# Optimization experiments

Hardware: AMD Instinct MI355X
Metric: run time of the kernel (lower is better)

The kernel has to match this reference:

```python
import jax, jax.numpy as jnp
import numpy as np

B, T, C, H = 2, 2048, 1024, 16
HD = C // H  # head_size = 64
EPS = 1e-5


def setup_inputs() -> dict:
    key = jax.random.key(0)
    ks = jax.random.split(key, 12)
    s = lambda fan_in: 1.0 / np.sqrt(fan_in)
    return {
        "x": jax.random.normal(ks[0], (B, T, C), jnp.float32),
        # attention projections, stored [in, out] so y = x @ W
        "Wq": jax.random.normal(ks[1], (C, C), jnp.float32) * s(C),
        "Wk": jax.random.normal(ks[2], (C, C), jnp.float32) * s(C),
        "Wv": jax.random.normal(ks[3], (C, C), jnp.float32) * s(C),
        "Wo": jax.random.normal(ks[4], (C, C), jnp.float32) * s(C),
        "bo": jnp.zeros((C,), jnp.float32),
        "ln1_g": jnp.ones((C,), jnp.float32),
        "ln1_b": jnp.zeros((C,), jnp.float32),
        "ln2_g": jnp.ones((C,), jnp.float32),
        "ln2_b": jnp.zeros((C,), jnp.float32),
        "W1": jax.random.normal(ks[5], (C, 4 * C), jnp.float32) * s(C),
        "b1": jnp.zeros((4 * C,), jnp.float32),
        "W2": jax.random.normal(ks[6], (4 * C, C), jnp.float32) * s(4 * C),
        "b2": jnp.zeros((C,), jnp.float32),
    }


def _layernorm(x, g, b):
    mu = jnp.mean(x, axis=-1, keepdims=True)
    var = jnp.mean(jnp.square(x - mu), axis=-1, keepdims=True)
    return (x - mu) * jax.lax.rsqrt(var + EPS) * g + b


def reference(x, Wq, Wk, Wv, Wo, bo, ln1_g, ln1_b, ln2_g, ln2_b, W1, b1, W2, b2):
    # Dropout layers are inference no-ops (eval mode).
    Bz, Tz, Cz = x.shape
    h = _layernorm(x, ln1_g, ln1_b)
    # fused multi-head projections (equivalent to per-head Linears concatenated)
    q = (h @ Wq).reshape(Bz, Tz, H, HD)
    k = (h @ Wk).reshape(Bz, Tz, H, HD)
    v = (h @ Wv).reshape(Bz, Tz, H, HD)
    scores = jnp.einsum("bqhd,bkhd->bhqk", q, k) / np.sqrt(HD).astype(np.float32)
    causal = jnp.tril(jnp.ones((Tz, Tz), bool))
    scores = jnp.where(causal, scores, -jnp.inf)
    attn = jax.nn.softmax(scores, axis=-1)
    out = jnp.einsum("bhqk,bkhd->bqhd", attn, v).reshape(Bz, Tz, Cz)
    x = x + out @ Wo + bo
    h2 = _layernorm(x, ln2_g, ln2_b)
    ff = jax.nn.relu(h2 @ W1 + b1) @ W2 + b2
    return x + ff
```

## Files before the change

kernel.cpp:

```cpp
#include <hip/hip_runtime.h>
#include <hip/hip_bf16.h>
#include <stdint.h>

#define B_  2
#define T_  2048
#define C_  1024
#define H_  16
#define HD_ 64
#define M_  4096
#define FF_ 4096

typedef unsigned short ushort_t;
typedef __bf16 bf16x8 __attribute__((ext_vector_type(8)));
typedef float  f32x4  __attribute__((ext_vector_type(4)));

__device__ inline ushort_t f2bf(float f) {
  uint32_t u = __builtin_bit_cast(uint32_t, f);
  u += 0x7fffu + ((u >> 16) & 1u);
  return (ushort_t)(u >> 16);
}

__device__ inline void gload_lds16(const void* g, void* l) {
  __builtin_amdgcn_global_load_lds(
      (const __attribute__((address_space(1))) uint32_t*)g,
      (__attribute__((address_space(3))) uint32_t*)l, 16, 0, 0);
}

__device__ inline int qswz(int row, int byte_in_row) {
  return row * 128 + (byte_in_row ^ ((row & 7) << 4));
}
__device__ inline int vswz(int row, int byte_in_row) {
  return row * 128 + (byte_in_row ^ (((row >> 3) & 7) << 4));
}

__global__ __launch_bounds__(256) void lnorm_kernel(
    const float* __restrict__ x, const float* __restrict__ g,
    const float* __restrict__ b, ushort_t* __restrict__ o) {
  int row = blockIdx.x;
  int tid = threadIdx.x;
  const float4* xr = (const float4*)(x + (size_t)row * C_);
  float4 xv = xr[tid];
  float s  = xv.x + xv.y + xv.z + xv.w;
  float s2 = xv.x*xv.x + xv.y*xv.y + xv.z*xv.z + xv.w*xv.w;
#pragma unroll
  for (int off = 32; off; off >>= 1) {
    s  += __shfl_down(s,  off);
    s2 += __shfl_down(s2, off);
  }
  __shared__ float rs[4], rq[4];
  int wid = tid >> 6;
  if ((tid & 63) == 0) { rs[wid] = s; rq[wid] = s2; }
  __syncthreads();
  float tot  = rs[0] + rs[1] + rs[2] + rs[3];
  float tot2 = rq[0] + rq[1] + rq[2] + rq[3];
  float mu   = tot * (1.0f / C_);
  float var  = tot2 * (1.0f / C_) - mu * mu;
  float rstd = rsqrtf(var + 1e-5f);
  float4 gv = ((const float4*)g)[tid];
  float4 bv = ((const float4*)b)[tid];
  float y0 = (xv.x - mu) * rstd * gv.x + bv.x;
  float y1 = (xv.y - mu) * rstd * gv.y + bv.y;
  float y2 = (xv.z - mu) * rstd * gv.z + bv.z;
  float y3 = (xv.w - mu) * rstd * gv.w + bv.w;
  uint2 pk;
  pk.x = (uint32_t)f2bf(y0) | ((uint32_t)f2bf(y1) << 16);
  pk.y = (uint32_t)f2bf(y2) | ((uint32_t)f2bf(y3) << 16);
  *(uint2*)(o + (size_t)row * C_ + tid * 4) = pk;
}

__global__ __launch_bounds__(256) void tcast_kernel(
    const float* __restrict__ W, ushort_t* __restrict__ Wt, int K, int N) {
  __shared__ float t[32][33];
  int bn = blockIdx.x, bk = blockIdx.y;
  int tx = threadIdx.x & 31, ty = threadIdx.x >> 5;
#pragma unroll
  for (int i = 0; i < 4; ++i)
    t[ty + i*8][tx] = W[(size_t)(bk*32 + ty + i*8) * N + bn*32 + tx];
  __syncthreads();
#pragma unroll
  for (int i = 0; i < 4; ++i)
    Wt[(size_t)(bn*32 + ty + i*8) * K + bk*32 + tx] = f2bf(t[tx][ty + i*8]);
}

template<int BIAS, int RELU, int RESID, int OUTBF16>
__global__ __launch_bounds__(256) void gemm_kernel(
    const ushort_t* __restrict__ A, const ushort_t* __restrict__ Bt,
    const float* __restrict__ bias, const float* __restrict__ resid,
    void* __restrict__ outp, int M, int N, int K) {
  __shared__ __align__(16) ushort_t As[128*32];
  __shared__ __align__(16) ushort_t Bs[128*32];
  int bn = blockIdx.x, bm = blockIdx.y;
  int tid = threadIdx.x;
  int lane = tid & 63, wid = tid >> 6;
  int wr = (wid >> 1) * 64, wc = (wid & 1) * 64;
  int r = lane & 15, g = lane >> 4;
  int srow = tid >> 2, scc = (tid & 3) * 8;
  int srow2 = srow + 64;
  f32x4 acc[4][4] = {};
  int nk = K >> 5;
  for (int kt = 0; kt < nk; ++kt) {
    gload_lds16(&A[(size_t)(bm*128 + srow)  * K + kt*32 + scc], &As[tid*8]);
    gload_lds16(&A[(size_t)(bm*128 + srow2) * K + kt*32 + scc], &As[(tid+256)*8]);
    gload_lds16(&Bt[(size_t)(bn*128 + srow)  * K + kt*32 + scc], &Bs[tid*8]);
    gload_lds16(&Bt[(size_t)(bn*128 + srow2) * K + kt*32 + scc], &Bs[(tid+256)*8]);
    __syncthreads();
    bf16x8 af[4], bfv[4];
#pragma unroll
    for (int m = 0; m < 4; ++m)
      af[m] = *(const bf16x8*)&As[(wr + m*16 + r)*32 + g*8];
#pragma unroll
    for (int n = 0; n < 4; ++n)
      bfv[n] = *(const bf16x8*)&Bs[(wc + n*16 + r)*32 + g*8];
#pragma unroll
    for (int m = 0; m < 4; ++m)
#pragma unroll
      for (int n = 0; n < 4; ++n)
        acc[m][n] = __builtin_amdgcn_mfma_f32_16x16x32_bf16(
            af[m], bfv[n], acc[m][n], 0, 0, 0);
    __syncthreads();
  }
#pragma unroll
  for (int m = 0; m < 4; ++m)
#pragma unroll
    for (int n = 0; n < 4; ++n)
#pragma unroll
      for (int e = 0; e < 4; ++e) {
        int row = bm*128 + wr + m*16 + g*4 + e;
        int col = bn*128 + wc + n*16 + r;
        float v = acc[m][n][e];
        if (BIAS)  v += bias[col];
        if (RESID) v += resid[(size_t)row * N + col];
        if (RELU)  v = fmaxf(v, 0.0f);
        if (OUTBF16) ((ushort_t*)outp)[(size_t)row * N + col] = f2bf(v);
        else         ((float*)outp)[(size_t)row * N + col]    = v;
      }
}

__global__ __launch_bounds__(256) void attn_kernel(
    const ushort_t* __restrict__ q, const ushort_t* __restrict__ k,
    const ushort_t* __restrict__ v, ushort_t* __restrict__ o, int ldq) {
  int bid = blockIdx.x;
  int qb = 31 - (bid & 31);
  int hh = (bid >> 5) & 15;
  int bb = bid >> 9;
  __shared__ __align__(16) ushort_t Qs[64*64], Ks[64*64], Vt[64*64];
  __shared__ __align__(16) ushort_t Ps[4][16*64];
  int tid = threadIdx.x, lane = tid & 63, w = tid >> 6;
  int r = lane & 15, g = lane >> 4;
#pragma unroll
  for (int p = 0; p < 2; ++p) {
    int ci = p*256 + tid;
    int row = ci >> 3, c8 = (ci & 7) * 8;
    *(uint4*)((char*)Qs + qswz(row, c8*2)) =
        *(const uint4*)&q[((size_t)(bb*T_ + qb*64 + row))*ldq + hh*64 + c8];
  }
  f32x4 O[4] = {};
  float mrow[4], lrow[4];
#pragma unroll
  for (int e = 0; e < 4; ++e) { mrow[e] = -1e30f; lrow[e] = 0.f; }
  for (int kb = 0; kb <= qb; ++kb) {
    __syncthreads();
#pragma unroll
    for (int p = 0; p < 2; ++p) {
      int ci = p*256 + tid;
      int row = ci >> 3, c8 = (ci & 7) * 8;
      *(uint4*)((char*)Ks + qswz(row, c8*2)) =
          *(const uint4*)&k[((size_t)(bb*T_ + kb*64 + row))*ldq + hh*64 + c8];
      int key = row;
      uint4 vv = *(const uint4*)&v[((size_t)(bb*T_ + kb*64 + key))*ldq + hh*64 + c8];
      ushort_t tmp[8];
      *(uint4*)tmp = vv;
#pragma unroll
      for (int j = 0; j < 8; ++j)
        *(ushort_t*)((char*)Vt + vswz(c8 + j, key*2)) = tmp[j];
    }
    __syncthreads();
    f32x4 s[4] = {};
#pragma unroll
    for (int ks = 0; ks < 2; ++ks) {
      bf16x8 aq = *(const bf16x8*)((char*)Qs + qswz(w*16 + r, (ks*32 + g*8)*2));
#pragma unroll
      for (int n = 0; n < 4; ++n) {
        bf16x8 bk = *(const bf16x8*)((char*)Ks + qswz(n*16 + r, (ks*32 + g*8)*2));
        s[n] = __builtin_amdgcn_mfma_f32_16x16x32_bf16(aq, bk, s[n], 0, 0, 0);
      }
    }
    int qrow0 = qb*64 + w*16 + g*4;
#pragma unroll
    for (int e = 0; e < 4; ++e) {
      float mx = -1e30f;
#pragma unroll
      for (int n = 0; n < 4; ++n) {
        float sv = s[n][e] * 0.125f;
        if (kb*64 + n*16 + r > qrow0 + e) sv = -1e30f;
        s[n][e] = sv;
        mx = fmaxf(mx, sv);
      }
#pragma unroll
      for (int off = 1; off < 16; off <<= 1)
        mx = fmaxf(mx, __shfl_xor(mx, off, 16));
      float mnew = fmaxf(mrow[e], mx);
      float sf = __expf(mrow[e] - mnew);
      mrow[e] = mnew;
      float rsum = 0.f;
#pragma unroll
      for (int n = 0; n < 4; ++n) {
        float p = __expf(s[n][e] - mnew);
        rsum += p;
        *(ushort_t*)((char*)&Ps[w][0] + qswz(g*4 + e, (n*16 + r)*2)) = f2bf(p);
      }
#pragma unroll
      for (int off = 1; off < 16; off <<= 1)
        rsum += __shfl_xor(rsum, off, 16);
      lrow[e] = lrow[e] * sf + rsum;
#pragma unroll
      for (int dn = 0; dn < 4; ++dn) O[dn][e] *= sf;
    }
    __syncthreads();
#pragma unroll
    for (int ks = 0; ks < 2; ++ks) {
      bf16x8 ap = *(const bf16x8*)((char*)&Ps[w][0] + qswz(r, (ks*32 + g*8)*2));
#pragma unroll
      for (int dn = 0; dn < 4; ++dn) {
        bf16x8 bv = *(const bf16x8*)((char*)Vt + vswz(dn*16 + r, (ks*32 + g*8)*2));
        O[dn] = __builtin_amdgcn_mfma_f32_16x16x32_bf16(ap, bv, O[dn], 0, 0, 0);
      }
    }
  }
#pragma unroll
  for (int dn = 0; dn < 4; ++dn)
#pragma unroll
    for (int e = 0; e < 4; ++e) {
      int tok = qb*64 + w*16 + g*4 + e;
      int col = hh*64 + dn*16 + r;
      o[((size_t)(bb*T_ + tok))*C_ + col] = f2bf(O[dn][e] / lrow[e]);
    }
}

extern "C" void kernel_launch(void* const* d_in, const int* in_sizes, int n_in,
                              void* d_out, int out_size, void* d_ws, size_t ws_size,
                              hipStream_t stream) {
  const float* x    = (const float*)d_in[0];
  const float* Wq   = (const float*)d_in[1];
  const float* Wk   = (const float*)d_in[2];
  const float* Wv   = (const float*)d_in[3];
  const float* Wo   = (const float*)d_in[4];
  const float* bo   = (const float*)d_in[5];
  const float* ln1g = (const float*)d_in[6];
  const float* ln1b = (const float*)d_in[7];
  const float* ln2g = (const float*)d_in[8];
  const float* ln2b = (const float*)d_in[9];
  const float* W1   = (const float*)d_in[10];
  const float* b1   = (const float*)d_in[11];
  const float* W2   = (const float*)d_in[12];
  const float* b2   = (const float*)d_in[13];

  char* ws = (char*)d_ws;
  ushort_t* h    = (ushort_t*)(ws + ((size_t)0  << 20));
  ushort_t* qkv  = (ushort_t*)(ws + ((size_t)8  << 20));
  ushort_t* ff   = (ushort_t*)(ws + ((size_t)0  << 20));
  ushort_t* attn = (ushort_t*)(ws + ((size_t)32 << 20));
  float*    x2   = (float*)   (ws + ((size_t)40 << 20));
  ushort_t* h2   = (ushort_t*)(ws + ((size_t)56 << 20));
  ushort_t* wqt  = (ushort_t*)(ws + ((size_t)64 << 20));
  ushort_t* wkt  = (ushort_t*)(ws + ((size_t)66 << 20));
  ushort_t* wvt  = (ushort_t*)(ws + ((size_t)68 << 20));
  ushort_t* wot  = (ushort_t*)(ws + ((size_t)70 << 20));
  ushort_t* w1t  = (ushort_t*)(ws + ((size_t)72 << 20));
  ushort_t* w2t  = (ushort_t*)(ws + ((size_t)80 << 20));
  float* out = (float*)d_out;

  tcast_kernel<<<dim3(32, 32),  256, 0, stream>>>(Wq, wqt, 1024, 1024);
  tcast_kernel<<<dim3(32, 32),  256, 0, stream>>>(Wk, wkt, 1024, 1024);
  tcast_kernel<<<dim3(32, 32),  256, 0, stream>>>(Wv, wvt, 1024, 1024);
  tcast_kernel<<<dim3(32, 32),  256, 0, stream>>>(Wo, wot, 1024, 1024);
  tcast_kernel<<<dim3(128, 32), 256, 0, stream>>>(W1, w1t, 1024, 4096);
  tcast_kernel<<<dim3(32, 128), 256, 0, stream>>>(W2, w2t, 4096, 1024);

  lnorm_kernel<<<M_, 256, 0, stream>>>(x, ln1g, ln1b, h);

  gemm_kernel<0,0,0,1><<<dim3(24, 32), 256, 0, stream>>>(h, wqt, nullptr, nullptr, qkv, M_, 3*C_, C_);

  attn_kernel<<<B_*H_*(T_/64), 256, 0, stream>>>(qkv, qkv + C_, qkv + 2*C_, attn, 3*C_);

  gemm_kernel<1,0,1,0><<<dim3(8, 32), 256, 0, stream>>>(attn, wot, bo, x, x2, M_, C_, C_);

  lnorm_kernel<<<M_, 256, 0, stream>>>(x2, ln2g, ln2b, h2);

  gemm_kernel<1,1,0,1><<<dim3(32, 32), 256, 0, stream>>>(h2, w1t, b1, nullptr, ff, M_, FF_, C_);

  gemm_kernel<1,0,1,0><<<dim3(8, 32), 256, 0, stream>>>(ff, w2t, b2, x2, out, M_, C_, FF_);
}
```

Before: 493.4 us.

## Restructure attention with 128-key tiles, pre-transposed V, register prefetch

Adds a separate kernel that transposes V into a head-major [d][token] buffer, so the attention kernel can load V with vector stores instead of scalar transposed LDS writes. The attention kernel now processes 128-key tiles and prefetches the next K/V tile into registers while computing the current one. It also keeps Q fragments in registers, applies the causal mask only on the last tile, folds the softmax scale into exp2, and computes row sums with an MFMA against a ones vector instead of shuffle reductions. This adds an extra kernel launch and a global round trip for V, and uses more LDS and registers per block.

```diff
diff --git a/kernel.cpp b/kernel.cpp
--- a/kernel.cpp
+++ b/kernel.cpp
@@ -9,10 +9,13 @@
 #define HD_ 64
 #define M_  4096
 #define FF_ 4096
+#define KV_ 128
 
 typedef unsigned short ushort_t;
 typedef __bf16 bf16x8 __attribute__((ext_vector_type(8)));
 typedef float  f32x4  __attribute__((ext_vector_type(4)));
+
+#define C2_ 0.1803368801111204f
 
 __device__ inline ushort_t f2bf(float f) {
   uint32_t u = __builtin_bit_cast(uint32_t, f);
@@ -29,8 +32,10 @@
 __device__ inline int qswz(int row, int byte_in_row) {
   return row * 128 + (byte_in_row ^ ((row & 7) << 4));
 }
-__device__ inline int vswz(int row, int byte_in_row) {
-  return row * 128 + (byte_in_row ^ (((row >> 3) & 7) << 4));
+__device__ inline int swz256(int row, int byte_in_row) {
+  int slot = byte_in_row >> 4;
+  int sl = slot ^ ((row & 3) << 2) ^ ((row >> 2) & 3);
+  return row * 256 + sl * 16 + (byte_in_row & 15);
 }
 
 __global__ __launch_bounds__(256) void lnorm_kernel(
@@ -80,6 +85,28 @@
 #pragma unroll
   for (int i = 0; i < 4; ++i)
     Wt[(size_t)(bn*32 + ty + i*8) * K + bk*32 + tx] = f2bf(t[tx][ty + i*8]);
+}
+
+__global__ __launch_bounds__(256) void vtrans_kernel(
+    const ushort_t* __restrict__ qkv, ushort_t* __restrict__ vt) {
+  __shared__ ushort_t t[32][33];
+  int tt = blockIdx.x;
+  int cc = blockIdx.y;
+  int bb = blockIdx.z;
+  int tx = threadIdx.x & 31, ty = threadIdx.x >> 5;
+#pragma unroll
+  for (int i = 0; i < 4; ++i)
+    t[ty + i*8][tx] = qkv[(size_t)(bb*T_ + tt*32 + ty + i*8)*3072 + 2048 + cc*32 + tx];
+  __syncthreads();
+  int crow = threadIdx.x >> 4;
+  int ucol = threadIdx.x & 15;
+#pragma unroll
+  for (int i = 0; i < 2; ++i) {
+    int c = crow + i*16;
+    uint32_t vlo = t[ucol*2][c], vhi = t[ucol*2 + 1][c];
+    *(uint32_t*)&vt[(size_t)(bb*1024 + cc*32 + c)*T_ + tt*32 + ucol*2] =
+        vlo | (vhi << 16);
+  }
 }
 
 template<int BIAS, int RELU, int RESID, int OUTBF16>
@@ -138,15 +165,18 @@
 
 __global__ __launch_bounds__(256) void attn_kernel(
     const ushort_t* __restrict__ q, const ushort_t* __restrict__ k,
-    const ushort_t* __restrict__ v, ushort_t* __restrict__ o, int ldq) {
+    const ushort_t* __restrict__ vt, ushort_t* __restrict__ o, int ldq) {
   int bid = blockIdx.x;
   int qb = 31 - (bid & 31);
   int hh = (bid >> 5) & 15;
   int bb = bid >> 9;
-  __shared__ __align__(16) ushort_t Qs[64*64], Ks[64*64], Vt[64*64];
-  __shared__ __align__(16) ushort_t Ps[4][16*64];
+  __shared__ __align__(16) ushort_t Qs[64*64];
+  __shared__ __align__(16) ushort_t Ks[128*64];
+  __shared__ __align__(16) ushort_t Vts[64*128];
+  __shared__ __align__(16) ushort_t Ps[4][16*128];
   int tid = threadIdx.x, lane = tid & 63, w = tid >> 6;
   int r = lane & 15, g = lane >> 4;
+
 #pragma unroll
   for (int p = 0; p < 2; ++p) {
     int ci = p*256 + tid;
@@ -154,79 +184,119 @@
     *(uint4*)((char*)Qs + qswz(row, c8*2)) =
         *(const uint4*)&q[((size_t)(bb*T_ + qb*64 + row))*ldq + hh*64 + c8];
   }
+  __syncthreads();
+  bf16x8 aq[2];
+#pragma unroll
+  for (int ks = 0; ks < 2; ++ks)
+    aq[ks] = *(const bf16x8*)((char*)Qs + qswz(w*16 + r, (ks*32 + g*8)*2));
+
+  bf16x8 onesv;
+#pragma unroll
+  for (int j = 0; j < 8; ++j) onesv[j] = (__bf16)1.0f;
+
   f32x4 O[4] = {};
   float mrow[4], lrow[4];
 #pragma unroll
   for (int e = 0; e < 4; ++e) { mrow[e] = -1e30f; lrow[e] = 0.f; }
-  for (int kb = 0; kb <= qb; ++kb) {
+
+  int nkv = (qb*64 + 64 + KV_ - 1) / KV_;
+
+  const ushort_t* kbase = k  + (size_t)bb*T_*ldq + hh*64;
+  const ushort_t* vbase = vt + (size_t)((bb*H_ + hh)*HD_) * T_;
+  uint4 kreg[4], vreg[4];
+  int krow0 = tid >> 3, kslot = tid & 7;
+  int vrow0 = tid >> 4, vslot = tid & 15;
+
+#pragma unroll
+  for (int i = 0; i < 4; ++i)
+    kreg[i] = *(const uint4*)(kbase + (size_t)(krow0 + i*32)*ldq + kslot*8);
+#pragma unroll
+  for (int i = 0; i < 4; ++i)
+    vreg[i] = *(const uint4*)(vbase + (size_t)(vrow0 + i*16)*T_ + vslot*8);
+
+  for (int kt = 0; kt < nkv; ++kt) {
     __syncthreads();
 #pragma unroll
-    for (int p = 0; p < 2; ++p) {
-      int ci = p*256 + tid;
-      int row = ci >> 3, c8 = (ci & 7) * 8;
-      *(uint4*)((char*)Ks + qswz(row, c8*2)) =
-          *(const uint4*)&k[((size_t)(bb*T_ + kb*64 + row))*ldq + hh*64 + c8];
-      int key = row;
-      uint4 vv = *(const uint4*)&v[((size_t)(bb*T_ + kb*64 + key))*ldq + hh*64 + c8];
-      ushort_t tmp[8];
-      *(uint4*)tmp = vv;
-#pragma unroll
-      for (int j = 0; j < 8; ++j)
-        *(ushort_t*)((char*)Vt + vswz(c8 + j, key*2)) = tmp[j];
+    for (int i = 0; i < 4; ++i) {
+      int row = krow0 + i*32;
+      *(uint4*)((char*)Ks + row*128 + ((kslot*16) ^ ((row & 7) << 4))) = kreg[i];
+    }
+#pragma unroll
+    for (int i = 0; i < 4; ++i) {
+      int d = vrow0 + i*16;
+      int sl = vslot ^ ((d & 3) << 2) ^ ((d >> 2) & 3);
+      *(uint4*)((char*)Vts + d*256 + sl*16) = vreg[i];
     }
     __syncthreads();
-    f32x4 s[4] = {};
-#pragma unroll
-    for (int ks = 0; ks < 2; ++ks) {
-      bf16x8 aq = *(const bf16x8*)((char*)Qs + qswz(w*16 + r, (ks*32 + g*8)*2));
-#pragma unroll
-      for (int n = 0; n < 4; ++n) {
+    if (kt + 1 < nkv) {
+#pragma unroll
+      for (int i = 0; i < 4; ++i)
+        kreg[i] = *(const uint4*)(kbase + (size_t)((kt+1)*KV_ + krow0 + i*32)*ldq + kslot*8);
+#pragma unroll
+      for (int i = 0; i < 4; ++i)
+        vreg[i] = *(const uint4*)(vbase + (size_t)(vrow0 + i*16)*T_ + (kt+1)*KV_ + vslot*8);
+    }
+
+    f32x4 s[8];
+#pragma unroll
+    for (int n = 0; n < 8; ++n) s[n] = (f32x4){0.f, 0.f, 0.f, 0.f};
+#pragma unroll
+    for (int ks = 0; ks < 2; ++ks)
+#pragma unroll
+      for (int n = 0; n < 8; ++n) {
         bf16x8 bk = *(const bf16x8*)((char*)Ks + qswz(n*16 + r, (ks*32 + g*8)*2));
-        s[n] = __builtin_amdgcn_mfma_f32_16x16x32_bf16(aq, bk, s[n], 0, 0, 0);
-      }
-    }
-    int qrow0 = qb*64 + w*16 + g*4;
+        s[n] = __builtin_amdgcn_mfma_f32_16x16x32_bf16(aq[ks], bk, s[n], 0, 0, 0);
+      }
+
+    bool lastt = (kt == nkv - 1);
 #pragma unroll
     for (int e = 0; e < 4; ++e) {
       float mx = -1e30f;
-#pragma unroll
-      for (int n = 0; n < 4; ++n) {
-        float sv = s[n][e] * 0.125f;
-        if (kb*64 + n*16 + r > qrow0 + e) sv = -1e30f;
-        s[n][e] = sv;
-        mx = fmaxf(mx, sv);
+      if (lastt) {
+        int qrow = qb*64 + w*16 + g*4 + e;
+#pragma unroll
+        for (int n = 0; n < 8; ++n) {
+          float sv = s[n][e];
+          if (kt*KV_ + n*16 + r > qrow) sv = -1e30f;
+          s[n][e] = sv;
+          mx = fmaxf(mx, sv);
+        }
+      } else {
+#pragma unroll
+        for (int n = 0; n < 8; ++n) mx = fmaxf(mx, s[n][e]);
       }
 #pragma unroll
       for (int off = 1; off < 16; off <<= 1)
         mx = fmaxf(mx, __shfl_xor(mx, off, 16));
       float mnew = fmaxf(mrow[e], mx);
-      float sf = __expf(mrow[e] - mnew);
+      float sfe = exp2f((mrow[e] - mnew) * C2_);
       mrow[e] = mnew;
-      float rsum = 0.f;
-#pragma unroll
-      for (int n = 0; n < 4; ++n) {
-        float p = __expf(s[n][e] - mnew);
-        rsum += p;
-        *(ushort_t*)((char*)&Ps[w][0] + qswz(g*4 + e, (n*16 + r)*2)) = f2bf(p);
-      }
-#pragma unroll
-      for (int off = 1; off < 16; off <<= 1)
-        rsum += __shfl_xor(rsum, off, 16);
-      lrow[e] = lrow[e] * sf + rsum;
-#pragma unroll
-      for (int dn = 0; dn < 4; ++dn) O[dn][e] *= sf;
-    }
-    __syncthreads();
-#pragma unroll
-    for (int ks = 0; ks < 2; ++ks) {
-      bf16x8 ap = *(const bf16x8*)((char*)&Ps[w][0] + qswz(r, (ks*32 + g*8)*2));
+      float mc = mnew * C2_;
+#pragma unroll
+      for (int n = 0; n < 8; ++n) {
+        float p = exp2f(s[n][e] * C2_ - mc);
+        *(ushort_t*)((char*)&Ps[w][0] + swz256(g*4 + e, (n*16 + r)*2)) = f2bf(p);
+      }
+      lrow[e] *= sfe;
+#pragma unroll
+      for (int dn = 0; dn < 4; ++dn) O[dn][e] *= sfe;
+    }
+
+    f32x4 sums = (f32x4){0.f, 0.f, 0.f, 0.f};
+#pragma unroll
+    for (int ks2 = 0; ks2 < 4; ++ks2) {
+      bf16x8 ap = *(const bf16x8*)((char*)&Ps[w][0] + swz256(r, ks2*64 + g*16));
+      sums = __builtin_amdgcn_mfma_f32_16x16x32_bf16(ap, onesv, sums, 0, 0, 0);
 #pragma unroll
       for (int dn = 0; dn < 4; ++dn) {
-        bf16x8 bv = *(const bf16x8*)((char*)Vt + vswz(dn*16 + r, (ks*32 + g*8)*2));
+        bf16x8 bv = *(const bf16x8*)((char*)Vts + swz256(dn*16 + r, ks2*64 + g*16));
         O[dn] = __builtin_amdgcn_mfma_f32_16x16x32_bf16(ap, bv, O[dn], 0, 0, 0);
       }
     }
-  }
+#pragma unroll
+    for (int e = 0; e < 4; ++e) lrow[e] += sums[e];
+  }
+
 #pragma unroll
   for (int dn = 0; dn < 4; ++dn)
 #pragma unroll
@@ -257,6 +327,7 @@
 
   char* ws = (char*)d_ws;
   ushort_t* h    = (ushort_t*)(ws + ((size_t)0  << 20));
+  ushort_t* vt   = (ushort_t*)(ws + ((size_t)0  << 20));
   ushort_t* qkv  = (ushort_t*)(ws + ((size_t)8  << 20));
   ushort_t* ff   = (ushort_t*)(ws + ((size_t)0  << 20));
   ushort_t* attn = (ushort_t*)(ws + ((size_t)32 << 20));
@@ -281,7 +352,9 @@
 
   gemm_kernel<0,0,0,1><<<dim3(24, 32), 256, 0, stream>>>(h, wqt, nullptr, nullptr, qkv, M_, 3*C_, C_);
 
-  attn_kernel<<<B_*H_*(T_/64), 256, 0, stream>>>(qkv, qkv + C_, qkv + 2*C_, attn, 3*C_);
+  vtrans_kernel<<<dim3(64, 32, 2), 256, 0, stream>>>(qkv, vt);
+
+  attn_kernel<<<B_*H_*(T_/64), 256, 0, stream>>>(qkv, qkv + C_, vt, attn, 3*C_);
 
   gemm_kernel<1,0,1,0><<<dim3(8, 32), 256, 0, stream>>>(attn, wot, bo, x, x2, M_, C_, C_);
 
```

Result: slower. 520.1 us (+5.4%).

## Rewrite attention with 32x32 MFMA, register-resident Q/P, pre-transposed V

Applied to the files above, without the earlier changes.

Attention now processes 128 query rows per block, with each wave owning 32 query rows. It uses 32x32x16 bf16 MFMAs that compute S^T, so Q stays in registers and the P operand is built by lane shuffles instead of round-tripping through LDS. A separate kernel pre-transposes V into a [B, C, T] buffer so K and V^T tiles can be fetched with direct global-to-LDS loads, replacing the per-element scalar transpose stores. Softmax uses exp2 with a folded scale. The cost is an extra launch and an extra V write and read, plus some waves idling on tiles beyond their causal limit.

```diff
diff --git a/kernel.cpp b/kernel.cpp
--- a/kernel.cpp
+++ b/kernel.cpp
@@ -13,12 +13,20 @@
 typedef unsigned short ushort_t;
 typedef __bf16 bf16x8 __attribute__((ext_vector_type(8)));
 typedef float  f32x4  __attribute__((ext_vector_type(4)));
+typedef float  f32x16 __attribute__((ext_vector_type(16)));
+typedef unsigned int u32x2 __attribute__((ext_vector_type(2)));
+typedef unsigned int u32x4 __attribute__((ext_vector_type(4)));
+
+#define C2_ 0.1803368801111204f
 
 __device__ inline ushort_t f2bf(float f) {
   uint32_t u = __builtin_bit_cast(uint32_t, f);
   u += 0x7fffu + ((u >> 16) & 1u);
   return (ushort_t)(u >> 16);
 }
+__device__ inline uint32_t pk2(float lo, float hi) {
+  return (uint32_t)f2bf(lo) | ((uint32_t)f2bf(hi) << 16);
+}
 
 __device__ inline void gload_lds16(const void* g, void* l) {
   __builtin_amdgcn_global_load_lds(
@@ -28,9 +36,6 @@
 
 __device__ inline int qswz(int row, int byte_in_row) {
   return row * 128 + (byte_in_row ^ ((row & 7) << 4));
-}
-__device__ inline int vswz(int row, int byte_in_row) {
-  return row * 128 + (byte_in_row ^ (((row >> 3) & 7) << 4));
 }
 
 __global__ __launch_bounds__(256) void lnorm_kernel(
@@ -80,6 +85,28 @@
 #pragma unroll
   for (int i = 0; i < 4; ++i)
     Wt[(size_t)(bn*32 + ty + i*8) * K + bk*32 + tx] = f2bf(t[tx][ty + i*8]);
+}
+
+__global__ __launch_bounds__(256) void vtrans_kernel(
+    const ushort_t* __restrict__ qkv, ushort_t* __restrict__ vt) {
+  __shared__ ushort_t t[32][33];
+  int tt = blockIdx.x;
+  int cc = blockIdx.y;
+  int bb = blockIdx.z;
+  int tx = threadIdx.x & 31, ty = threadIdx.x >> 5;
+#pragma unroll
+  for (int i = 0; i < 4; ++i)
+    t[ty + i*8][tx] = qkv[(size_t)(bb*T_ + tt*32 + ty + i*8)*3072 + 2048 + cc*32 + tx];
+  __syncthreads();
+  int crow = threadIdx.x >> 4;
+  int ucol = threadIdx.x & 15;
+#pragma unroll
+  for (int i = 0; i < 2; ++i) {
+    int c = crow + i*16;
+    uint32_t vlo = t[ucol*2][c], vhi = t[ucol*2 + 1][c];
+    *(uint32_t*)&vt[(size_t)(bb*1024 + cc*32 + c)*T_ + tt*32 + ucol*2] =
+        vlo | (vhi << 16);
+  }
 }
 
 template<int BIAS, int RELU, int RESID, int OUTBF16>
@@ -138,103 +165,122 @@
 
 __global__ __launch_bounds__(256) void attn_kernel(
     const ushort_t* __restrict__ q, const ushort_t* __restrict__ k,
-    const ushort_t* __restrict__ v, ushort_t* __restrict__ o, int ldq) {
+    const ushort_t* __restrict__ vt, ushort_t* __restrict__ o, int ldq) {
   int bid = blockIdx.x;
-  int qb = 31 - (bid & 31);
-  int hh = (bid >> 5) & 15;
-  int bb = bid >> 9;
-  __shared__ __align__(16) ushort_t Qs[64*64], Ks[64*64], Vt[64*64];
-  __shared__ __align__(16) ushort_t Ps[4][16*64];
+  int qbb = 15 - (bid & 15);
+  int hh = (bid >> 4) & 15;
+  int bb = bid >> 8;
+  __shared__ __align__(16) ushort_t Ks[64*64];
+  __shared__ __align__(16) ushort_t Vts[64*64];
   int tid = threadIdx.x, lane = tid & 63, w = tid >> 6;
-  int r = lane & 15, g = lane >> 4;
-#pragma unroll
-  for (int p = 0; p < 2; ++p) {
-    int ci = p*256 + tid;
-    int row = ci >> 3, c8 = (ci & 7) * 8;
-    *(uint4*)((char*)Qs + qswz(row, c8*2)) =
-        *(const uint4*)&q[((size_t)(bb*T_ + qb*64 + row))*ldq + hh*64 + c8];
-  }
-  f32x4 O[4] = {};
-  float mrow[4], lrow[4];
-#pragma unroll
-  for (int e = 0; e < 4; ++e) { mrow[e] = -1e30f; lrow[e] = 0.f; }
-  for (int kb = 0; kb <= qb; ++kb) {
+  int qi = lane & 31, hi = lane >> 5;
+  int qrow0 = qbb*128 + w*32;
+  int qg = qrow0 + qi;
+  int lt = 2*qbb + (w >> 1);
+  int nkv = 2*qbb + 2;
+
+  const ushort_t* qbase = q + ((size_t)(bb*T_ + qg))*ldq + hh*64;
+  bf16x8 qv[4];
+#pragma unroll
+  for (int c = 0; c < 4; ++c)
+    qv[c] = *(const bf16x8*)(qbase + c*16 + hi*8);
+
+  const ushort_t* kbase = k  + ((size_t)bb*T_)*ldq + hh*64;
+  const ushort_t* vbase = vt + ((size_t)(bb*1024 + hh*64))*T_;
+
+  int r0s = tid >> 3;
+  int s0  = ((tid & 7) ^ (r0s & 7)) * 8;
+
+  f32x16 O0 = {}, O1 = {};
+  float mrun = -1e30f, lrun = 0.f;
+
+  for (int kt = 0; kt < nkv; ++kt) {
+    gload_lds16(kbase + ((size_t)(kt*64 + r0s))*ldq + s0,      &Ks[tid*8]);
+    gload_lds16(kbase + ((size_t)(kt*64 + r0s + 32))*ldq + s0, &Ks[(tid+256)*8]);
+    gload_lds16(vbase + (size_t)r0s*T_ + kt*64 + s0,           &Vts[tid*8]);
+    gload_lds16(vbase + (size_t)(r0s+32)*T_ + kt*64 + s0,      &Vts[(tid+256)*8]);
     __syncthreads();
-#pragma unroll
-    for (int p = 0; p < 2; ++p) {
-      int ci = p*256 + tid;
-      int row = ci >> 3, c8 = (ci & 7) * 8;
-      *(uint4*)((char*)Ks + qswz(row, c8*2)) =
-          *(const uint4*)&k[((size_t)(bb*T_ + kb*64 + row))*ldq + hh*64 + c8];
-      int key = row;
-      uint4 vv = *(const uint4*)&v[((size_t)(bb*T_ + kb*64 + key))*ldq + hh*64 + c8];
-      ushort_t tmp[8];
-      *(uint4*)tmp = vv;
-#pragma unroll
-      for (int j = 0; j < 8; ++j)
-        *(ushort_t*)((char*)Vt + vswz(c8 + j, key*2)) = tmp[j];
+    if (kt <= lt) {
+      f32x16 a0 = {}, a1 = {};
+#pragma unroll
+      for (int c = 0; c < 4; ++c) {
+        bf16x8 k0 = *(const bf16x8*)((char*)Ks + qswz(qi,      c*32 + hi*16));
+        bf16x8 k1 = *(const bf16x8*)((char*)Ks + qswz(32 + qi, c*32 + hi*16));
+        a0 = __builtin_amdgcn_mfma_f32_32x32x16_bf16(k0, qv[c], a0, 0, 0, 0);
+        a1 = __builtin_amdgcn_mfma_f32_32x32x16_bf16(k1, qv[c], a1, 0, 0, 0);
+      }
+      if (kt == lt) {
+        int kof = kt*64 + 4*hi;
+#pragma unroll
+        for (int rg = 0; rg < 16; ++rg) {
+          int kp = kof + (rg & 3) + 8*(rg >> 2);
+          if (kp > qg)      a0[rg] = -1e30f;
+          if (kp + 32 > qg) a1[rg] = -1e30f;
+        }
+      }
+      float tm = -1e30f;
+#pragma unroll
+      for (int rg = 0; rg < 16; ++rg) tm = fmaxf(tm, fmaxf(a0[rg], a1[rg]));
+      tm = fmaxf(tm, __shfl_xor(tm, 32));
+      float mnew = fmaxf(mrun, tm);
+      float sf = exp2f((mrun - mnew) * C2_);
+      mrun = mnew;
+      float mc = mnew * C2_;
+#pragma unroll
+      for (int rg = 0; rg < 16; ++rg) {
+        a0[rg] = exp2f(a0[rg]*C2_ - mc);
+        a1[rg] = exp2f(a1[rg]*C2_ - mc);
+      }
+      float rs = 0.f;
+#pragma unroll
+      for (int rg = 0; rg < 16; ++rg) rs += a0[rg] + a1[rg];
+      rs += __shfl_xor(rs, 32);
+      lrun = lrun*sf + rs;
+#pragma unroll
+      for (int rg = 0; rg < 16; ++rg) { O0[rg] *= sf; O1[rg] *= sf; }
+      bf16x8 pf[4];
+#pragma unroll
+      for (int kb = 0; kb < 2; ++kb)
+#pragma unroll
+        for (int jj = 0; jj < 2; ++jj) {
+          int rb = jj*8;
+          float v0 = kb ? a1[rb+0] : a0[rb+0], v1 = kb ? a1[rb+1] : a0[rb+1];
+          float v2 = kb ? a1[rb+2] : a0[rb+2], v3 = kb ? a1[rb+3] : a0[rb+3];
+          float v4 = kb ? a1[rb+4] : a0[rb+4], v5 = kb ? a1[rb+5] : a0[rb+5];
+          float v6 = kb ? a1[rb+6] : a0[rb+6], v7 = kb ? a1[rb+7] : a0[rb+7];
+          uint32_t d0 = pk2(v0, v1), d1 = pk2(v2, v3);
+          uint32_t e0 = pk2(v4, v5), e1 = pk2(v6, v7);
+          uint32_t pd0 = __shfl_xor(d0, 32), pd1 = __shfl_xor(d1, 32);
+          uint32_t pe0 = __shfl_xor(e0, 32), pe1 = __shfl_xor(e1, 32);
+          u32x4 fw;
+          fw[0] = hi ? pe0 : d0;
+          fw[1] = hi ? pe1 : d1;
+          fw[2] = hi ? e0  : pd0;
+          fw[3] = hi ? e1  : pd1;
+          pf[kb*2 + jj] = __builtin_bit_cast(bf16x8, fw);
+        }
+#pragma unroll
+      for (int kk = 0; kk < 4; ++kk) {
+        bf16x8 vv0 = *(const bf16x8*)((char*)Vts + qswz(qi,      kk*32 + hi*16));
+        bf16x8 vv1 = *(const bf16x8*)((char*)Vts + qswz(32 + qi, kk*32 + hi*16));
+        O0 = __builtin_amdgcn_mfma_f32_32x32x16_bf16(vv0, pf[kk], O0, 0, 0, 0);
+        O1 = __builtin_amdgcn_mfma_f32_32x32x16_bf16(vv1, pf[kk], O1, 0, 0, 0);
+      }
     }
     __syncthreads();
-    f32x4 s[4] = {};
-#pragma unroll
-    for (int ks = 0; ks < 2; ++ks) {
-      bf16x8 aq = *(const bf16x8*)((char*)Qs + qswz(w*16 + r, (ks*32 + g*8)*2));
-#pragma unroll
-      for (int n = 0; n < 4; ++n) {
-        bf16x8 bk = *(const bf16x8*)((char*)Ks + qswz(n*16 + r, (ks*32 + g*8)*2));
-        s[n] = __builtin_amdgcn_mfma_f32_16x16x32_bf16(aq, bk, s[n], 0, 0, 0);
-      }
-    }
-    int qrow0 = qb*64 + w*16 + g*4;
-#pragma unroll
-    for (int e = 0; e < 4; ++e) {
-      float mx = -1e30f;
-#pragma unroll
-      for (int n = 0; n < 4; ++n) {
-        float sv = s[n][e] * 0.125f;
-        if (kb*64 + n*16 + r > qrow0 + e) sv = -1e30f;
-        s[n][e] = sv;
-        mx = fmaxf(mx, sv);
-      }
-#pragma unroll
-      for (int off = 1; off < 16; off <<= 1)
-        mx = fmaxf(mx, __shfl_xor(mx, off, 16));
-      float mnew = fmaxf(mrow[e], mx);
-      float sf = __expf(mrow[e] - mnew);
-      mrow[e] = mnew;
-      float rsum = 0.f;
-#pragma unroll
-      for (int n = 0; n < 4; ++n) {
-        float p = __expf(s[n][e] - mnew);
-        rsum += p;
-        *(ushort_t*)((char*)&Ps[w][0] + qswz(g*4 + e, (n*16 + r)*2)) = f2bf(p);
-      }
-#pragma unroll
-      for (int off = 1; off < 16; off <<= 1)
-        rsum += __shfl_xor(rsum, off, 16);
-      lrow[e] = lrow[e] * sf + rsum;
-#pragma unroll
-      for (int dn = 0; dn < 4; ++dn) O[dn][e] *= sf;
-    }
-    __syncthreads();
-#pragma unroll
-    for (int ks = 0; ks < 2; ++ks) {
-      bf16x8 ap = *(const bf16x8*)((char*)&Ps[w][0] + qswz(r, (ks*32 + g*8)*2));
-#pragma unroll
-      for (int dn = 0; dn < 4; ++dn) {
-        bf16x8 bv = *(const bf16x8*)((char*)Vt + vswz(dn*16 + r, (ks*32 + g*8)*2));
-        O[dn] = __builtin_amdgcn_mfma_f32_16x16x32_bf16(ap, bv, O[dn], 0, 0, 0);
-      }
-    }
-  }
-#pragma unroll
-  for (int dn = 0; dn < 4; ++dn)
-#pragma unroll
-    for (int e = 0; e < 4; ++e) {
-      int tok = qb*64 + w*16 + g*4 + e;
-      int col = hh*64 + dn*16 + r;
-      o[((size_t)(bb*T_ + tok))*C_ + col] = f2bf(O[dn][e] / lrow[e]);
-    }
+  }
+  float inv = 1.0f / lrun;
+  ushort_t* ob = o + ((size_t)(bb*T_ + qg))*C_ + hh*64;
+#pragma unroll
+  for (int tq = 0; tq < 4; ++tq) {
+    u32x2 st0, st1;
+    st0[0] = pk2(O0[4*tq+0]*inv, O0[4*tq+1]*inv);
+    st0[1] = pk2(O0[4*tq+2]*inv, O0[4*tq+3]*inv);
+    st1[0] = pk2(O1[4*tq+0]*inv, O1[4*tq+1]*inv);
+    st1[1] = pk2(O1[4*tq+2]*inv, O1[4*tq+3]*inv);
+    *(u32x2*)(ob + 8*tq + 4*hi)      = st0;
+    *(u32x2*)(ob + 32 + 8*tq + 4*hi) = st1;
+  }
 }
 
 extern "C" void kernel_launch(void* const* d_in, const int* in_sizes, int n_in,
@@ -257,6 +303,7 @@
 
   char* ws = (char*)d_ws;
   ushort_t* h    = (ushort_t*)(ws + ((size_t)0  << 20));
+  ushort_t* vt   = (ushort_t*)(ws + ((size_t)0  << 20));
   ushort_t* qkv  = (ushort_t*)(ws + ((size_t)8  << 20));
   ushort_t* ff   = (ushort_t*)(ws + ((size_t)0  << 20));
   ushort_t* attn = (ushort_t*)(ws + ((size_t)32 << 20));
@@ -281,7 +328,9 @@
 
   gemm_kernel<0,0,0,1><<<dim3(24, 32), 256, 0, stream>>>(h, wqt, nullptr, nullptr, qkv, M_, 3*C_, C_);
 
-  attn_kernel<<<B_*H_*(T_/64), 256, 0, stream>>>(qkv, qkv + C_, qkv + 2*C_, attn, 3*C_);
+  vtrans_kernel<<<dim3(64, 32, 2), 256, 0, stream>>>(qkv, vt);
+
+  attn_kernel<<<512, 256, 0, stream>>>(qkv, qkv + C_, vt, attn, 3*C_);
 
   gemm_kernel<1,0,1,0><<<dim3(8, 32), 256, 0, stream>>>(attn, wot, bo, x, x2, M_, C_, C_);
 
```

Result: faster. 457.0 us (-7.4%).
